# Kernel tuning notes

Hardware: AMD Instinct MI355X
Metric: run time of the kernel (lower is better)

Reference implementation:

```python
import jax, jax.numpy as jnp
import numpy as np

B, S, D, H, KV, HD = 2, 2048, 4096, 32, 8, 128
N_REP = H // KV


def _rope(t, fr, fi):
    # t: [b, s, h, hd]; fr/fi: [s, hd//2] broadcast as [1, s, 1, hd//2]
    t2 = t.reshape(*t.shape[:-1], -1, 2)
    tr, ti = t2[..., 0], t2[..., 1]
    fr = fr[None, :, None, :]
    fi = fi[None, :, None, :]
    orr = tr * fr - fi * ti
    oi = tr * fi + ti * fr
    return jnp.stack([orr, oi], axis=-1).reshape(t.shape)


def setup_inputs() -> dict:
    key = jax.random.key(0)
    ks = jax.random.split(key, 8)
    scale = 0.02
    x = jax.random.normal(ks[0], (B, S, D), jnp.float32)
    wq = jax.random.normal(ks[1], (H * HD, D), jnp.float32) * scale
    wk = jax.random.normal(ks[2], (KV * HD, D), jnp.float32) * scale
    wv = jax.random.normal(ks[3], (KV * HD, D), jnp.float32) * scale
    wo = jax.random.normal(ks[4], (D, H * HD), jnp.float32) * scale
    # rotary frequencies (real/imag parts of freqs_cis)
    t = jnp.arange(S, dtype=jnp.float32)
    inv = 1.0 / (10000.0 ** (jnp.arange(0, HD, 2, dtype=jnp.float32) / HD))
    ang = t[:, None] * inv[None, :]  # [S, HD//2]
    fr, fi = jnp.cos(ang), jnp.sin(ang)
    # causal mask, additive
    mask = jnp.triu(jnp.full((S, S), -1e9, jnp.float32), 1)[None, None]
    cache_k = jnp.zeros((B, S, KV, HD), jnp.float32)
    cache_v = jnp.zeros((B, S, KV, HD), jnp.float32)
    indexes = jnp.arange(S, dtype=jnp.int32)
    cache_indexes = jnp.arange(S, dtype=jnp.int32)
    return dict(x=x, wq=wq, wk=wk, wv=wv, wo=wo, fr=fr, fi=fi, mask=mask,
                cache_k=cache_k, cache_v=cache_v, indexes=indexes,
                cache_indexes=cache_indexes)


def reference(x, wq, wk, wv, wo, fr, fi, mask, cache_k, cache_v, indexes, cache_indexes):
    bsz, seqlen, _ = x.shape
    xq = jnp.einsum('bsd,ed->bse', x, wq).reshape(bsz, seqlen, H, HD)
    xk = jnp.einsum('bsd,ed->bse', x, wk).reshape(bsz, seqlen, KV, HD)
    xv = jnp.einsum('bsd,ed->bse', x, wv).reshape(bsz, seqlen, KV, HD)
    xq = _rope(xq, fr, fi)
    xk = _rope(xk, fr, fi)
    # KV-cache scatter then gather
    cache_k = cache_k.at[:, indexes].set(xk)
    cache_v = cache_v.at[:, indexes].set(xv)
    keys = cache_k[:, cache_indexes]    # [b, kv_len, KV, hd]
    values = cache_v[:, cache_indexes]
    # GQA: repeat_interleave kv heads
    keys = jnp.repeat(keys, N_REP, axis=2)      # [b, kv_len, H, hd]
    values = jnp.repeat(values, N_REP, axis=2)
    q = xq.transpose(0, 2, 1, 3)        # [b, H, s, hd]
    k = keys.transpose(0, 2, 1, 3)      # [b, H, kv, hd]
    v = values.transpose(0, 2, 1, 3)
    scores = jnp.einsum('bhqd,bhkd->bhqk', q, k) / jnp.sqrt(jnp.float32(HD))
    scores = scores + mask
    probs = jax.nn.softmax(scores.astype(jnp.float32), axis=-1).astype(q.dtype)
    out = jnp.einsum('bhqk,bhkd->bhqd', probs, v)
    out = out.transpose(0, 2, 1, 3).reshape(bsz, seqlen, H * HD)
    out = jnp.einsum('bse,de->bsd', out, wo)
    return (out, xk, xv)
```

## Files before the change

### kernel.cpp

```cpp
#include <hip/hip_runtime.h>
#include <hip/hip_bf16.h>


typedef __attribute__((ext_vector_type(8)))  short s8v;
typedef __attribute__((ext_vector_type(4)))  short s4v;
typedef __attribute__((ext_vector_type(4)))  float f4v;
typedef __attribute__((ext_vector_type(16))) float f16v;
typedef __attribute__((ext_vector_type(2)))  float f2v;
typedef __attribute__((ext_vector_type(2))) unsigned int u2v;
typedef __attribute__((ext_vector_type(4))) unsigned int u4v;

typedef __attribute__((address_space(3))) void lds_void;
typedef __attribute__((address_space(1))) void g_void;

#define GLDS16(gp, lp) __builtin_amdgcn_global_load_lds((g_void*)(gp), (lds_void*)(lp), 16, 0, 0)

#define SCL_LOG2 0.12751744f

__device__ __forceinline__ unsigned short f2b(float f) {
  unsigned u = __builtin_bit_cast(unsigned, f);
  u += 0x7fffu + ((u >> 16) & 1u);
  return (unsigned short)(u >> 16);
}
__device__ __forceinline__ unsigned pk2(float a, float b) {
  return (unsigned)f2b(a) | ((unsigned)f2b(b) << 16);
}
__device__ __forceinline__ float b2f(unsigned short h) {
  return __builtin_bit_cast(float, (unsigned)h << 16);
}

__device__ __forceinline__ void mfma32(f4v& d, s8v a, s8v b) {
  asm volatile("v_mfma_f32_16x16x32_bf16 %0, %1, %2, %0" : "+v"(d) : "v"(a), "v"(b));
}
__device__ __forceinline__ void mfma3216(f16v& d, s8v a, s8v b) {
  asm volatile("v_mfma_f32_32x32x16_bf16 %0, %1, %2, %0" : "+v"(d) : "v"(a), "v"(b));
}
__device__ __forceinline__ s4v tr_read(const char* p, int imm) {
  s4v r;
  asm volatile("ds_read_b64_tr_b16 %0, %1 offset:%2"
               : "=v"(r) : "v"((lds_void*)p), "n"(imm));
  return r;
}

__global__ __launch_bounds__(256) void cvt_bf16(const float* __restrict__ s,
                                                unsigned short* __restrict__ d, int n4) {
  const int i = blockIdx.x * 256 + threadIdx.x;
  if (i >= n4) return;
  f4v v = *(const f4v*)(s + (size_t)i * 4);
  u2v r;
  r.x = pk2(v[0], v[1]);
  r.y = pk2(v[2], v[3]);
  *(u2v*)(d + (size_t)i * 4) = r;
}

#define BAR      asm volatile("s_barrier" ::: "memory")
#define WLGKM    do { asm volatile("s_waitcnt lgkmcnt(0)" ::: "memory"); \
                      __builtin_amdgcn_sched_barrier(0); } while (0)
#define WVM8     do { asm volatile("s_waitcnt vmcnt(8)" ::: "memory"); \
                      __builtin_amdgcn_sched_barrier(0); } while (0)

template <int OUTB>
__global__ __launch_bounds__(512, 2) void gemm_bt8(const unsigned short* __restrict__ A,
                                                   const unsigned short* __restrict__ Bp,
                                                   void* __restrict__ Cout,
                                                   int M, int N, int Ks, int Klen,
                                                   int nTiles) {
  __shared__ __align__(16) char smem[131072];
  const int tid = threadIdx.x, lane = tid & 63, wv = tid >> 6;
  const int qi = lane & 15, g = lane >> 4;
  const int wm = wv >> 2, wn = wv & 3;

  const int nwg = gridDim.x, cpx = nwg >> 3;
  const int id = blockIdx.x;
  const int swz = (id & 7) * cpx + (id >> 3);
  const int half = swz / nTiles;
  const int tile = swz - half * nTiles;
  const int kOff = half * Klen;
  const int MT = M >> 8;
  const int m0 = (tile % MT) * 256, n0 = (tile / MT) * 256;
  const int NT = Klen >> 6;

  const int srowo = wv * 8 + (lane >> 3);
  const int scole = ((lane & 7) ^ (lane >> 3)) << 3;
  const size_t rA = (size_t)(m0 + srowo) * Ks + kOff + scole;
  const size_t rB = (size_t)(n0 + srowo) * Ks + kOff + scole;
  char* sdA = smem + wv * 1024;
  char* sdB = smem + 32768 + wv * 1024;

#define STG_A(D, H, KT) do { \
    GLDS16(A + rA + (size_t)((H)*128) * Ks + (size_t)(KT)*64,      sdA + (D)*65536 + (H)*16384); \
    GLDS16(A + rA + (size_t)((H)*128 + 64) * Ks + (size_t)(KT)*64, sdA + (D)*65536 + (H)*16384 + 8192); } while (0)
#define STG_B(D, H, KT) do { \
    GLDS16(Bp + rB + (size_t)((H)*128) * Ks + (size_t)(KT)*64,      sdB + (D)*65536 + (H)*16384); \
    GLDS16(Bp + rB + (size_t)((H)*128 + 64) * Ks + (size_t)(KT)*64, sdB + (D)*65536 + (H)*16384 + 8192); } while (0)

  const int sw = (qi & 7) << 4;
  const char* frA = smem + (wm * 128 + qi) * 128;
  const char* frB = smem + 32768 + (wn * 64 + qi) * 128;

#define RDA4(D, F0) do { _Pragma("unroll") for (int f_ = 0; f_ < 4; ++f_) \
    _Pragma("unroll") for (int k_ = 0; k_ < 2; ++k_) \
      a[(F0) + f_][k_] = *(const s8v*)(frA + (D)*65536 + ((F0) + f_) * 2048 + (((k_ << 6) + (g << 4)) ^ sw)); } while (0)
#define RDB2(D, N0) do { _Pragma("unroll") for (int n_ = 0; n_ < 2; ++n_) \
    _Pragma("unroll") for (int k_ = 0; k_ < 2; ++k_) \
      b[(N0) + n_][k_] = *(const s8v*)(frB + (D)*65536 + ((N0) + n_) * 2048 + (((k_ << 6) + (g << 4)) ^ sw)); } while (0)
#define MQUAD(F0, N0) do { __builtin_amdgcn_s_setprio(1); \
    _Pragma("unroll") for (int f_ = 0; f_ < 4; ++f_) \
    _Pragma("unroll") for (int n_ = 0; n_ < 2; ++n_) \
    _Pragma("unroll") for (int k_ = 0; k_ < 2; ++k_) \
      mfma32(acc[(F0) + f_][(N0) + n_], a[(F0) + f_][k_], b[(N0) + n_][k_]); \
    __builtin_amdgcn_s_setprio(0); } while (0)

  f4v acc[8][4];
#pragma unroll
  for (int i = 0; i < 8; ++i)
#pragma unroll
    for (int j = 0; j < 4; ++j) acc[i][j] = (f4v)0.0f;

  STG_A(0, 0, 0); STG_A(0, 1, 0); STG_B(0, 0, 0); STG_B(0, 1, 0);
  STG_A(1, 0, 1); STG_A(1, 1, 1); STG_B(1, 0, 1); STG_B(1, 1, 1);
  WVM8;
  BAR;

  s8v a[8][2], b[4][2];
#pragma unroll 1
  for (int it = 0; it < NT / 2; ++it) {
    const int t = 2 * it;
    const int k2 = (t + 2 < NT) ? t + 2 : NT - 1;
    const int k3 = (t + 3 < NT) ? t + 3 : NT - 1;
    RDA4(0, 0); RDB2(0, 0);
    WLGKM; MQUAD(0, 0); BAR;
    RDB2(0, 2);
    WLGKM; MQUAD(0, 2); BAR;
    RDA4(0, 4);
    STG_B(0, 0, k2); STG_B(0, 1, k2);
    WLGKM; MQUAD(4, 0); BAR;
    STG_A(0, 0, k2); STG_A(0, 1, k2);
    MQUAD(4, 2);
    WVM8; BAR;
    RDA4(1, 0); RDB2(1, 0);
    WLGKM; MQUAD(0, 0); BAR;
    RDB2(1, 2);
    WLGKM; MQUAD(0, 2); BAR;
    RDA4(1, 4);
    STG_B(1, 0, k3); STG_B(1, 1, k3);
    WLGKM; MQUAD(4, 0); BAR;
    STG_A(1, 0, k3); STG_A(1, 1, k3);
    MQUAD(4, 2);
    WVM8; BAR;
  }

  asm volatile("s_waitcnt vmcnt(0)" ::: "memory");
  asm volatile("s_nop 7\n\ts_nop 7" ::: "memory");
  const int r4 = g * 4;
  if (OUTB) {
    unsigned short* Cb = (unsigned short*)Cout + (size_t)half * M * N;
#pragma unroll
    for (int fm = 0; fm < 8; ++fm)
#pragma unroll
      for (int fn = 0; fn < 4; ++fn)
#pragma unroll
        for (int r = 0; r < 4; ++r)
          Cb[(size_t)(m0 + wm * 128 + fm * 16 + r4 + r) * N + (n0 + wn * 64 + fn * 16 + qi)] =
              f2b(acc[fm][fn][r]);
  } else {
    float* Cf = (float*)Cout;
#pragma unroll
    for (int fm = 0; fm < 8; ++fm)
#pragma unroll
      for (int fn = 0; fn < 4; ++fn)
#pragma unroll
        for (int r = 0; r < 4; ++r)
          Cf[(size_t)(m0 + wm * 128 + fm * 16 + r4 + r) * N + (n0 + wn * 64 + fn * 16 + qi)] =
              acc[fm][fn][r];
  }
}

__global__ __launch_bounds__(256) void rope_scatter(
    const unsigned short* __restrict__ qkvp, const float* __restrict__ fr,
    const float* __restrict__ fi,
    unsigned short* __restrict__ qb, unsigned short* __restrict__ kb,
    unsigned short* __restrict__ vbuf, float* __restrict__ xk, float* __restrict__ xv) {
  const int idx = blockIdx.x * 256 + threadIdx.x;
  const int token = idx / 3072;
  const int col2  = (idx - token * 3072) * 2;
  const int pos   = token & 2047;
  const unsigned u1 = *(const unsigned*)(qkvp + (size_t)token * 6144 + col2);
  const unsigned u2 = *(const unsigned*)(qkvp + 25165824u + (size_t)token * 6144 + col2);
  float v0 = b2f((unsigned short)u1) + b2f((unsigned short)u2);
  float v1 = b2f((unsigned short)(u1 >> 16)) + b2f((unsigned short)(u2 >> 16));
  if (col2 < 4096) {
    const int j = (col2 & 127) >> 1;
    const float cr = fr[pos * 64 + j], ci = fi[pos * 64 + j];
    const float a = (v0 * cr - ci * v1) * SCL_LOG2;
    const float o = (v0 * ci + v1 * cr) * SCL_LOG2;
    *(unsigned*)(qb + (size_t)token * 4096 + col2) = pk2(a, o);
  } else if (col2 < 5120) {
    const int lc = col2 - 4096;
    const int j = (lc & 127) >> 1;
    const float cr = fr[pos * 64 + j], ci = fi[pos * 64 + j];
    const float a = v0 * cr - ci * v1;
    const float o = v0 * ci + v1 * cr;
    *(unsigned*)(kb + (size_t)token * 1024 + lc) = pk2(a, o);
    f2v w; w.x = a; w.y = o;
    *(f2v*)(xk + (size_t)token * 1024 + lc) = w;
  } else {
    const int lc = col2 - 5120;
    *(unsigned*)(vbuf + (size_t)token * 1024 + lc) = pk2(v0, v1);
    f2v w; w.x = v0; w.y = v1;
    *(f2v*)(xv + (size_t)token * 1024 + lc) = w;
  }
}

__global__ __launch_bounds__(512, 2) void attn_fwd(
    const unsigned short* __restrict__ qb, const unsigned short* __restrict__ kb,
    const unsigned short* __restrict__ vb, unsigned short* __restrict__ ao) {
  __shared__ __align__(16) char smem[81920];
  const int tid = threadIdx.x, lane = tid & 63, wv = tid >> 6;
  const int q31 = lane & 31, hi = lane >> 5;
  const int qtb = 7 - blockIdx.x;
  const int h = blockIdx.y, b = blockIdx.z, kvh = h >> 2;
  const int q0 = qtb * 256;
  const int qrow = q0 + wv * 32 + q31;

  s8v qf[8];
  {
    const unsigned short* qp = qb + (size_t)(b * 2048 + qrow) * 4096 + h * 128 + hi * 8;
#pragma unroll
    for (int c = 0; c < 8; ++c) qf[c] = *(const s8v*)(qp + c * 16);
  }

  f16v oacc[4];
#pragma unroll
  for (int i = 0; i < 4; ++i) oacc[i] = (f16v)0.0f;
  float m_run = -3.0e38f, l_run = 0.0f;

  const unsigned short* ksrc[2]; int kdo[2];
#pragma unroll
  for (int j = 0; j < 2; ++j) {
    const int r = wv * 8 + j * 4 + (lane >> 4);
    ksrc[j] = kb + (size_t)(b * 2048 + r) * 1024 + kvh * 128 + (((lane & 15) ^ (r & 15)) << 3);
    kdo[j] = (wv * 8 + j * 4) * 256;
  }
  const unsigned short* vsrc[2]; int vdo[2];
#pragma unroll
  for (int j = 0; j < 2; ++j) {
    const int key = (wv * 2 + j) * 4 + ((lane & 7) >> 1);
    const int d = ((lane >> 3) & 7) * 16 + (lane & 1) * 8;
    vsrc[j] = vb + (size_t)(b * 2048 + key) * 1024 + kvh * 128 + d;
    vdo[j] = (wv * 16 + j * 8) * 128;
  }

  const int ntiles = 4 * qtb + 4;
  const int my_qmax = q0 + wv * 32 + 31, wq_lo = q0 + wv * 32;

  GLDS16(ksrc[0], smem + kdo[0]);
  GLDS16(ksrc[1], smem + kdo[1]);
  GLDS16(ksrc[0] + 65536, smem + 16384 + kdo[0]);
  GLDS16(ksrc[1] + 65536, smem + 16384 + kdo[1]);
  GLDS16(vsrc[0], smem + 49152 + vdo[0]);
  GLDS16(vsrc[1], smem + 49152 + vdo[1]);
  asm volatile("s_waitcnt vmcnt(4)" ::: "memory");
  __builtin_amdgcn_sched_barrier(0);
  BAR;

  int kc = 0;
  for (int t = 0; t < ntiles; ++t) {
    const int k0 = t * 64;
    const bool live = (k0 <= my_qmax);
    const char* Kbase = smem + kc * 16384;
    f16v s32a = (f16v)0.0f, s32b = (f16v)0.0f;
    if (live) {
      __builtin_amdgcn_s_setprio(1);
#pragma unroll
      for (int c = 0; c < 8; ++c) {
        const int sl = ((2 * c + hi) ^ (q31 & 15)) << 4;
        s8v kfa = *(const s8v*)(Kbase + q31 * 256 + sl);
        s8v kfb = *(const s8v*)(Kbase + (32 + q31) * 256 + sl);
        mfma3216(s32a, kfa, qf[c]);
        mfma3216(s32b, kfb, qf[c]);
      }
      __builtin_amdgcn_s_setprio(0);
      asm volatile("s_nop 7\n\ts_nop 7\n\ts_nop 7" : "+v"(s32a), "+v"(s32b));
    }
    {
      const int kt2 = (t + 2 < ntiles) ? t + 2 : ntiles - 1;
      char* kd = smem + ((kc >= 1) ? kc - 1 : 2) * 16384;
      GLDS16(ksrc[0] + (size_t)kt2 * 65536, kd + kdo[0]);
      GLDS16(ksrc[1] + (size_t)kt2 * 65536, kd + kdo[1]);
    }
    asm volatile("s_waitcnt vmcnt(2)" ::: "memory");
    __builtin_amdgcn_sched_barrier(0);
    BAR;
    if (live) {
      const char* vbt = smem + 49152 + (t & 1) * 16384 + hi * 2048 +
                        ((lane >> 4) & 1) * 128 + ((lane & 15) << 3);
      s4v tA[8], tB[8];
#pragma unroll
      for (int u = 0; u < 8; ++u) tA[u] = tr_read(vbt, (u >> 1) * 256 + (u & 1) * 1024);

      float p[32];
#pragma unroll
      for (int r = 0; r < 16; ++r) { p[r] = s32a[r]; p[16 + r] = s32b[r]; }
      float tm = -3.0e38f;
      if (k0 + 64 <= wq_lo) {
#pragma unroll
        for (int j = 0; j < 32; ++j) tm = fmaxf(tm, p[j]);
      } else {
#pragma unroll
        for (int j = 0; j < 32; ++j) {
          const int keyg = k0 + (j >> 4) * 32 + (j & 3) + 8 * ((j >> 2) & 3) + 4 * hi;
          p[j] = (keyg <= qrow) ? p[j] : -3.0e38f;
          tm = fmaxf(tm, p[j]);
        }
      }
      tm = fmaxf(tm, __shfl_xor(tm, 32));

      if (!__all(tm - m_run <= 8.0f)) {
        const float m_new = fmaxf(m_run, tm);
        const float al = exp2f(m_run - m_new);
#pragma unroll
        for (int i = 0; i < 4; ++i)
#pragma unroll
          for (int r = 0; r < 16; ++r) oacc[i][r] *= al;
        l_run *= al;
        m_run = m_new;
      }
      float ps = 0.0f;
#pragma unroll
      for (int j = 0; j < 32; ++j) { p[j] = exp2f(p[j] - m_run); ps += p[j]; }
      ps += __shfl_xor(ps, 32);
      l_run += ps;

      s8v pf[4];
#pragma unroll
      for (int ks = 0; ks < 4; ++ks) {
        unsigned c0, c1, c2, c3;
        asm("v_cvt_pk_bf16_f32 %0, %1, %2" : "=v"(c0) : "v"(p[ks*8+0]), "v"(p[ks*8+1]));
        asm("v_cvt_pk_bf16_f32 %0, %1, %2" : "=v"(c1) : "v"(p[ks*8+2]), "v"(p[ks*8+3]));
        asm("v_cvt_pk_bf16_f32 %0, %1, %2" : "=v"(c2) : "v"(p[ks*8+4]), "v"(p[ks*8+5]));
        asm("v_cvt_pk_bf16_f32 %0, %1, %2" : "=v"(c3) : "v"(p[ks*8+6]), "v"(p[ks*8+7]));
        asm volatile("v_permlane32_swap_b32 %0, %1" : "+v"(c0), "+v"(c2));
        asm volatile("v_permlane32_swap_b32 %0, %1" : "+v"(c1), "+v"(c3));
        u4v pw; pw.x = c0; pw.y = c1; pw.z = c2; pw.w = c3;
        pf[ks] = __builtin_bit_cast(s8v, pw);
      }

#define PVS(KS, CUR, NXT, LAST) do { \
        if (!(LAST)) { \
          _Pragma("unroll") for (int u = 0; u < 8; ++u) \
            NXT[u] = tr_read(vbt, ((KS)+1)*4096 + (u >> 1) * 256 + (u & 1) * 1024); \
          asm volatile("s_waitcnt lgkmcnt(8)" ::: "memory"); \
        } else { asm volatile("s_waitcnt lgkmcnt(0)" ::: "memory"); } \
        __builtin_amdgcn_sched_barrier(0); \
        __builtin_amdgcn_s_setprio(1); \
        _Pragma("unroll") for (int dt = 0; dt < 4; ++dt) { \
          s8v vf = __builtin_shufflevector(CUR[dt*2], CUR[dt*2+1], 0,1,2,3,4,5,6,7); \
          mfma3216(oacc[dt], vf, pf[KS]); } \
        __builtin_amdgcn_s_setprio(0); \
      } while (0)
      PVS(0, tA, tB, 0);
      PVS(1, tB, tA, 0);
      PVS(2, tA, tB, 0);
      PVS(3, tB, tA, 1);
#undef PVS
    }
    {
      const int vt1 = (t + 1 < ntiles) ? t + 1 : ntiles - 1;
      char* vd = smem + 49152 + ((t + 1) & 1) * 16384;
      GLDS16(vsrc[0] + (size_t)vt1 * 65536, vd + vdo[0]);
      GLDS16(vsrc[1] + (size_t)vt1 * 65536, vd + vdo[1]);
    }
    kc = (kc == 2) ? 0 : kc + 1;
  }

  asm volatile("s_waitcnt vmcnt(0) lgkmcnt(0)" ::: "memory");
  asm volatile("s_nop 7\n\ts_nop 7\n\ts_nop 7" ::: "memory");
  __syncthreads();
  const float inv = 1.0f / l_run;
  float* Ost = (float*)smem;
  const int er = tid >> 3, ew = (tid & 7) * 16;
#pragma unroll
  for (int pq = 0; pq < 4; ++pq) {
    if ((wv >> 1) == pq) {
      const int qip = (wv & 1) * 32 + q31;
#pragma unroll
      for (int dt = 0; dt < 4; ++dt)
#pragma unroll
        for (int r = 0; r < 16; ++r) {
          const int d = dt * 32 + (r & 3) + 8 * ((r >> 2) & 3) + 4 * hi;
          Ost[qip * 128 + (d ^ ((qip & 7) << 2))] = oacc[dt][r] * inv;
        }
    }
    __syncthreads();
    const int sw = (er & 7) << 2;
    f4v a0 = *(const f4v*)(Ost + er * 128 + ((ew + 0) ^ sw));
    f4v a1 = *(const f4v*)(Ost + er * 128 + ((ew + 4) ^ sw));
    f4v a2 = *(const f4v*)(Ost + er * 128 + ((ew + 8) ^ sw));
    f4v a3 = *(const f4v*)(Ost + er * 128 + ((ew + 12) ^ sw));
    u4v r0, r1;
    r0.x = pk2(a0[0], a0[1]); r0.y = pk2(a0[2], a0[3]);
    r0.z = pk2(a1[0], a1[1]); r0.w = pk2(a1[2], a1[3]);
    r1.x = pk2(a2[0], a2[1]); r1.y = pk2(a2[2], a2[3]);
    r1.z = pk2(a3[0], a3[1]); r1.w = pk2(a3[2], a3[3]);
    unsigned short* dst = ao + (size_t)(b * 2048 + q0 + pq * 64 + er) * 4096 + h * 128 + ew;
    *(u4v*)dst = r0;
    *(u4v*)(dst + 8) = r1;
    __syncthreads();
  }
}

extern "C" void kernel_launch(void* const* d_in, const int* in_sizes, int n_in,
                              void* d_out, int out_size, void* d_ws, size_t ws_size,
                              hipStream_t stream) {
  (void)in_sizes; (void)n_in; (void)out_size; (void)ws_size;
  const float* x  = (const float*)d_in[0];
  const float* wq = (const float*)d_in[1];
  const float* wk = (const float*)d_in[2];
  const float* wv = (const float*)d_in[3];
  const float* wo = (const float*)d_in[4];
  const float* fr = (const float*)d_in[5];
  const float* fi = (const float*)d_in[6];

  float* out = (float*)d_out;
  float* xk  = out + 16777216;
  float* xv  = xk + 4194304;

  char* ws = (char*)d_ws;
  unsigned short* xb    = (unsigned short*)(ws);
  unsigned short* wqkvb = (unsigned short*)(ws + 33554432);
  unsigned short* wob   = (unsigned short*)(ws + 83886080);
  unsigned short* qkvb  = (unsigned short*)(ws + 117440512);
  unsigned short* aob   = (unsigned short*)(ws + 117440512);
  unsigned short* qbuf  = (unsigned short*)(ws + 218103808);
  unsigned short* kbuf  = (unsigned short*)(ws + 251658240);
  unsigned short* vbuf  = (unsigned short*)(ws + 260046848);

  cvt_bf16<<<16384, 256, 0, stream>>>(x,  xb, 4194304);
  cvt_bf16<<<16384, 256, 0, stream>>>(wq, wqkvb, 4194304);
  cvt_bf16<<<4096,  256, 0, stream>>>(wk, wqkvb + 16777216, 1048576);
  cvt_bf16<<<4096,  256, 0, stream>>>(wv, wqkvb + 20971520, 1048576);
  cvt_bf16<<<16384, 256, 0, stream>>>(wo, wob, 4194304);

  gemm_bt8<1><<<768, 512, 0, stream>>>(xb, wqkvb, qkvb, 4096, 6144, 4096, 2048, 384);
  rope_scatter<<<49152, 256, 0, stream>>>(qkvb, fr, fi, qbuf, kbuf, vbuf, xk, xv);
  attn_fwd<<<dim3(8, 32, 2), 512, 0, stream>>>(qbuf, kbuf, vbuf, aob);
  gemm_bt8<0><<<256, 512, 0, stream>>>(aob, wob, out, 4096, 4096, 4096, 4096, 256);
}
```

Measured before the change: 596.5 us.

## Split causal attention KV range across two blocks and merge partials

Each query tile's key range is split into two halves, each handled by its own block, which doubles the attention grid. Each half writes an unnormalized bf16 partial output and its per-row max and sum. A new merge kernel combines the halves with log-sum-exp weights before the output projection. The aim is to even out the causal load imbalance, where late query tiles have far more key tiles, and to fill more CUs. The cost is an extra kernel launch, extra partial-output memory traffic, and some rounding from storing unnormalized partials in bf16.

Result: slower. 618.1 us (+3.6%).

```diff
diff --git a/kernel.cpp b/kernel.cpp
--- a/kernel.cpp
+++ b/kernel.cpp
@@ -214,14 +214,21 @@
 
 __global__ __launch_bounds__(512, 2) void attn_fwd(
     const unsigned short* __restrict__ qb, const unsigned short* __restrict__ kb,
-    const unsigned short* __restrict__ vb, unsigned short* __restrict__ ao) {
+    const unsigned short* __restrict__ vb, unsigned short* __restrict__ po,
+    float* __restrict__ st) {
   __shared__ __align__(16) char smem[81920];
   const int tid = threadIdx.x, lane = tid & 63, wv = tid >> 6;
   const int q31 = lane & 31, hi = lane >> 5;
-  const int qtb = 7 - blockIdx.x;
+  const int xx = blockIdx.x;
+  const int half = xx & 1;
+  const int qtb = 7 - (xx >> 1);
   const int h = blockIdx.y, b = blockIdx.z, kvh = h >> 2;
   const int q0 = qtb * 256;
   const int qrow = q0 + wv * 32 + q31;
+  const int nt_full = 4 * qtb + 4;
+  const int t0 = half ? (nt_full >> 1) : 0;
+  const int t1 = half ? nt_full : (nt_full >> 1);
+  unsigned short* pout = po + (size_t)half * 16777216u;
 
   s8v qf[8];
   {
@@ -251,21 +258,26 @@
     vdo[j] = (wv * 16 + j * 8) * 128;
   }
 
-  const int ntiles = 4 * qtb + 4;
   const int my_qmax = q0 + wv * 32 + 31, wq_lo = q0 + wv * 32;
 
-  GLDS16(ksrc[0], smem + kdo[0]);
-  GLDS16(ksrc[1], smem + kdo[1]);
-  GLDS16(ksrc[0] + 65536, smem + 16384 + kdo[0]);
-  GLDS16(ksrc[1] + 65536, smem + 16384 + kdo[1]);
-  GLDS16(vsrc[0], smem + 49152 + vdo[0]);
-  GLDS16(vsrc[1], smem + 49152 + vdo[1]);
+  {
+    const int tp1 = (t0 + 1 < t1) ? t0 + 1 : t1 - 1;
+    char* k0d = smem + (t0 % 3) * 16384;
+    char* k1d = smem + ((t0 + 1) % 3) * 16384;
+    char* v0d = smem + 49152 + (t0 & 1) * 16384;
+    GLDS16(ksrc[0] + (size_t)t0 * 65536, k0d + kdo[0]);
+    GLDS16(ksrc[1] + (size_t)t0 * 65536, k0d + kdo[1]);
+    GLDS16(ksrc[0] + (size_t)tp1 * 65536, k1d + kdo[0]);
+    GLDS16(ksrc[1] + (size_t)tp1 * 65536, k1d + kdo[1]);
+    GLDS16(vsrc[0] + (size_t)t0 * 65536, v0d + vdo[0]);
+    GLDS16(vsrc[1] + (size_t)t0 * 65536, v0d + vdo[1]);
+  }
   asm volatile("s_waitcnt vmcnt(4)" ::: "memory");
   __builtin_amdgcn_sched_barrier(0);
   BAR;
 
-  int kc = 0;
-  for (int t = 0; t < ntiles; ++t) {
+  int kc = t0 % 3;
+  for (int t = t0; t < t1; ++t) {
     const int k0 = t * 64;
     const bool live = (k0 <= my_qmax);
     const char* Kbase = smem + kc * 16384;
@@ -284,7 +296,7 @@
       asm volatile("s_nop 7\n\ts_nop 7\n\ts_nop 7" : "+v"(s32a), "+v"(s32b));
     }
     {
-      const int kt2 = (t + 2 < ntiles) ? t + 2 : ntiles - 1;
+      const int kt2 = (t + 2 < t1) ? t + 2 : t1 - 1;
       char* kd = smem + ((kc >= 1) ? kc - 1 : 2) * 16384;
       GLDS16(ksrc[0] + (size_t)kt2 * 65536, kd + kdo[0]);
       GLDS16(ksrc[1] + (size_t)kt2 * 65536, kd + kdo[1]);
@@ -366,7 +378,7 @@
 #undef PVS
     }
     {
-      const int vt1 = (t + 1 < ntiles) ? t + 1 : ntiles - 1;
+      const int vt1 = (t + 1 < t1) ? t + 1 : t1 - 1;
       char* vd = smem + 49152 + ((t + 1) & 1) * 16384;
       GLDS16(vsrc[0] + (size_t)vt1 * 65536, vd + vdo[0]);
       GLDS16(vsrc[1] + (size_t)vt1 * 65536, vd + vdo[1]);
@@ -374,10 +386,16 @@
     kc = (kc == 2) ? 0 : kc + 1;
   }
 
+  if (hi == 0) {
+    float* stp = st + (size_t)half * 262144;
+    const int row = (b * 2048 + q0 + wv * 32 + q31) * 32 + h;
+    f2v s; s.x = m_run; s.y = l_run;
+    *(f2v*)(stp + 2 * (size_t)row) = s;
+  }
+
   asm volatile("s_waitcnt vmcnt(0) lgkmcnt(0)" ::: "memory");
   asm volatile("s_nop 7\n\ts_nop 7\n\ts_nop 7" ::: "memory");
   __syncthreads();
-  const float inv = 1.0f / l_run;
   float* Ost = (float*)smem;
   const int er = tid >> 3, ew = (tid & 7) * 16;
 #pragma unroll
@@ -389,7 +407,7 @@
 #pragma unroll
         for (int r = 0; r < 16; ++r) {
           const int d = dt * 32 + (r & 3) + 8 * ((r >> 2) & 3) + 4 * hi;
-          Ost[qip * 128 + (d ^ ((qip & 7) << 2))] = oacc[dt][r] * inv;
+          Ost[qip * 128 + (d ^ ((qip & 7) << 2))] = oacc[dt][r];
         }
     }
     __syncthreads();
@@ -403,11 +421,38 @@
     r0.z = pk2(a1[0], a1[1]); r0.w = pk2(a1[2], a1[3]);
     r1.x = pk2(a2[0], a2[1]); r1.y = pk2(a2[2], a2[3]);
     r1.z = pk2(a3[0], a3[1]); r1.w = pk2(a3[2], a3[3]);
-    unsigned short* dst = ao + (size_t)(b * 2048 + q0 + pq * 64 + er) * 4096 + h * 128 + ew;
+    unsigned short* dst = pout + (size_t)(b * 2048 + q0 + pq * 64 + er) * 4096 + h * 128 + ew;
     *(u4v*)dst = r0;
     *(u4v*)(dst + 8) = r1;
     __syncthreads();
   }
+}
+
+__global__ __launch_bounds__(256) void attn_merge(
+    const unsigned short* __restrict__ po, const float* __restrict__ st,
+    unsigned short* __restrict__ ao) {
+  const int i = blockIdx.x * 256 + threadIdx.x;
+  const int dg = i & 15;
+  const int row = i >> 4;
+  const f2v s1 = *(const f2v*)(st + 2 * (size_t)row);
+  const f2v s2 = *(const f2v*)(st + 262144 + 2 * (size_t)row);
+  const float M = fmaxf(s1.x, s2.x);
+  const float w1 = exp2f(s1.x - M), w2 = exp2f(s2.x - M);
+  const float inv = 1.0f / (s1.y * w1 + s2.y * w2);
+  const int bq = row >> 5, h = row & 31;
+  const size_t off = (size_t)bq * 4096 + h * 128 + dg * 8;
+  u4v pa = *(const u4v*)(po + off);
+  u4v pb = *(const u4v*)(po + 16777216u + off);
+  u4v r;
+#pragma unroll
+  for (int w = 0; w < 4; ++w) {
+    const unsigned ua = ((unsigned*)&pa)[w], ub = ((unsigned*)&pb)[w];
+    const float lo = (b2f((unsigned short)ua) * w1 + b2f((unsigned short)ub) * w2) * inv;
+    const float hi = (b2f((unsigned short)(ua >> 16)) * w1 +
+                      b2f((unsigned short)(ub >> 16)) * w2) * inv;
+    ((unsigned*)&r)[w] = pk2(lo, hi);
+  }
+  *(u4v*)(ao + off) = r;
 }
 
 extern "C" void kernel_launch(void* const* d_in, const int* in_sizes, int n_in,
@@ -431,7 +476,9 @@
   unsigned short* wqkvb = (unsigned short*)(ws + 33554432);
   unsigned short* wob   = (unsigned short*)(ws + 83886080);
   unsigned short* qkvb  = (unsigned short*)(ws + 117440512);
-  unsigned short* aob   = (unsigned short*)(ws + 117440512);
+  unsigned short* part  = (unsigned short*)(ws + 117440512);
+  float*          stats = (float*)(ws + 188743680);
+  unsigned short* aob   = (unsigned short*)(ws);
   unsigned short* qbuf  = (unsigned short*)(ws + 218103808);
   unsigned short* kbuf  = (unsigned short*)(ws + 251658240);
   unsigned short* vbuf  = (unsigned short*)(ws + 260046848);
@@ -444,6 +491,7 @@
 
   gemm_bt8<1><<<768, 512, 0, stream>>>(xb, wqkvb, qkvb, 4096, 6144, 4096, 2048, 384);
   rope_scatter<<<49152, 256, 0, stream>>>(qkvb, fr, fi, qbuf, kbuf, vbuf, xk, xv);
-  attn_fwd<<<dim3(8, 32, 2), 512, 0, stream>>>(qbuf, kbuf, vbuf, aob);
+  attn_fwd<<<dim3(16, 32, 2), 512, 0, stream>>>(qbuf, kbuf, vbuf, part, stats);
+  attn_merge<<<8192, 256, 0, stream>>>(part, stats, aob);
   gemm_bt8<0><<<256, 512, 0, stream>>>(aob, wob, out, 4096, 4096, 4096, 4096, 256);
 }
```

## Halve attention query tile to 128 rows with 4-wave blocks

Applied to the files above, without the earlier changes.

Each attention block now covers 128 query rows with 4 waves instead of 256 rows with 8 waves, which doubles the grid to 16x32x2. Every wave issues twice as many K/V global-to-LDS loads per tile to keep the staging unchanged, and the epilogue writes 32 columns per thread. The goal is more blocks and better load balance across the causal triangle on the CUs, at the cost of more K/V reloads per query row and fewer waves to hide latency within a block.

Measured after the change: 578.8 us. 1.03x faster.

```diff
diff --git a/kernel.cpp b/kernel.cpp
--- a/kernel.cpp
+++ b/kernel.cpp
@@ -212,15 +212,15 @@
   }
 }
 
-__global__ __launch_bounds__(512, 2) void attn_fwd(
+__global__ __launch_bounds__(256, 2) void attn_fwd(
     const unsigned short* __restrict__ qb, const unsigned short* __restrict__ kb,
     const unsigned short* __restrict__ vb, unsigned short* __restrict__ ao) {
   __shared__ __align__(16) char smem[81920];
   const int tid = threadIdx.x, lane = tid & 63, wv = tid >> 6;
   const int q31 = lane & 31, hi = lane >> 5;
-  const int qtb = 7 - blockIdx.x;
+  const int qtb = 15 - blockIdx.x;
   const int h = blockIdx.y, b = blockIdx.z, kvh = h >> 2;
-  const int q0 = qtb * 256;
+  const int q0 = qtb * 128;
   const int qrow = q0 + wv * 32 + q31;
 
   s8v qf[8];
@@ -235,32 +235,37 @@
   for (int i = 0; i < 4; ++i) oacc[i] = (f16v)0.0f;
   float m_run = -3.0e38f, l_run = 0.0f;
 
-  const unsigned short* ksrc[2]; int kdo[2];
-#pragma unroll
-  for (int j = 0; j < 2; ++j) {
-    const int r = wv * 8 + j * 4 + (lane >> 4);
+  const unsigned short* ksrc[4]; int kdo[4];
+#pragma unroll
+  for (int j = 0; j < 4; ++j) {
+    const int r = wv * 16 + j * 4 + (lane >> 4);
     ksrc[j] = kb + (size_t)(b * 2048 + r) * 1024 + kvh * 128 + (((lane & 15) ^ (r & 15)) << 3);
-    kdo[j] = (wv * 8 + j * 4) * 256;
-  }
-  const unsigned short* vsrc[2]; int vdo[2];
-#pragma unroll
-  for (int j = 0; j < 2; ++j) {
-    const int key = (wv * 2 + j) * 4 + ((lane & 7) >> 1);
+    kdo[j] = (wv * 16 + j * 4) * 256;
+  }
+  const unsigned short* vsrc[4]; int vdo[4];
+#pragma unroll
+  for (int j = 0; j < 4; ++j) {
+    const int key = wv * 16 + j * 4 + ((lane & 7) >> 1);
     const int d = ((lane >> 3) & 7) * 16 + (lane & 1) * 8;
     vsrc[j] = vb + (size_t)(b * 2048 + key) * 1024 + kvh * 128 + d;
-    vdo[j] = (wv * 16 + j * 8) * 128;
-  }
-
-  const int ntiles = 4 * qtb + 4;
+    vdo[j] = (wv * 32 + j * 8) * 128;
+  }
+
+  const int ntiles = 2 * qtb + 2;
   const int my_qmax = q0 + wv * 32 + 31, wq_lo = q0 + wv * 32;
 
-  GLDS16(ksrc[0], smem + kdo[0]);
-  GLDS16(ksrc[1], smem + kdo[1]);
-  GLDS16(ksrc[0] + 65536, smem + 16384 + kdo[0]);
-  GLDS16(ksrc[1] + 65536, smem + 16384 + kdo[1]);
-  GLDS16(vsrc[0], smem + 49152 + vdo[0]);
-  GLDS16(vsrc[1], smem + 49152 + vdo[1]);
-  asm volatile("s_waitcnt vmcnt(4)" ::: "memory");
+  {
+    char* k0d = smem;
+    char* k1d = smem + 16384;
+    char* v0d = smem + 49152;
+#pragma unroll
+    for (int j = 0; j < 4; ++j) GLDS16(ksrc[j], k0d + kdo[j]);
+#pragma unroll
+    for (int j = 0; j < 4; ++j) GLDS16(ksrc[j] + 65536, k1d + kdo[j]);
+#pragma unroll
+    for (int j = 0; j < 4; ++j) GLDS16(vsrc[j], v0d + vdo[j]);
+  }
+  asm volatile("s_waitcnt vmcnt(8)" ::: "memory");
   __builtin_amdgcn_sched_barrier(0);
   BAR;
 
@@ -286,10 +291,10 @@
     {
       const int kt2 = (t + 2 < ntiles) ? t + 2 : ntiles - 1;
       char* kd = smem + ((kc >= 1) ? kc - 1 : 2) * 16384;
-      GLDS16(ksrc[0] + (size_t)kt2 * 65536, kd + kdo[0]);
-      GLDS16(ksrc[1] + (size_t)kt2 * 65536, kd + kdo[1]);
+#pragma unroll
+      for (int j = 0; j < 4; ++j) GLDS16(ksrc[j] + (size_t)kt2 * 65536, kd + kdo[j]);
     }
-    asm volatile("s_waitcnt vmcnt(2)" ::: "memory");
+    asm volatile("s_waitcnt vmcnt(4)" ::: "memory");
     __builtin_amdgcn_sched_barrier(0);
     BAR;
     if (live) {
@@ -368,8 +373,8 @@
     {
       const int vt1 = (t + 1 < ntiles) ? t + 1 : ntiles - 1;
       char* vd = smem + 49152 + ((t + 1) & 1) * 16384;
-      GLDS16(vsrc[0] + (size_t)vt1 * 65536, vd + vdo[0]);
-      GLDS16(vsrc[1] + (size_t)vt1 * 65536, vd + vdo[1]);
+#pragma unroll
+      for (int j = 0; j < 4; ++j) GLDS16(vsrc[j] + (size_t)vt1 * 65536, vd + vdo[j]);
     }
     kc = (kc == 2) ? 0 : kc + 1;
   }
@@ -379,10 +384,10 @@
   __syncthreads();
   const float inv = 1.0f / l_run;
   float* Ost = (float*)smem;
-  const int er = tid >> 3, ew = (tid & 7) * 16;
-#pragma unroll
-  for (int pq = 0; pq < 4; ++pq) {
-    if ((wv >> 1) == pq) {
+  const int er = tid >> 2, ew = (tid & 3) * 32;
+#pragma unroll
+  for (int p = 0; p < 2; ++p) {
+    if ((wv >> 1) == p) {
       const int qip = (wv & 1) * 32 + q31;
 #pragma unroll
       for (int dt = 0; dt < 4; ++dt)
@@ -394,18 +399,25 @@
     }
     __syncthreads();
     const int sw = (er & 7) << 2;
-    f4v a0 = *(const f4v*)(Ost + er * 128 + ((ew + 0) ^ sw));
-    f4v a1 = *(const f4v*)(Ost + er * 128 + ((ew + 4) ^ sw));
-    f4v a2 = *(const f4v*)(Ost + er * 128 + ((ew + 8) ^ sw));
-    f4v a3 = *(const f4v*)(Ost + er * 128 + ((ew + 12) ^ sw));
+    f4v av[8];
+#pragma unroll
+    for (int c = 0; c < 8; ++c)
+      av[c] = *(const f4v*)(Ost + er * 128 + ((ew + c * 4) ^ sw));
     u4v r0, r1;
-    r0.x = pk2(a0[0], a0[1]); r0.y = pk2(a0[2], a0[3]);
-    r0.z = pk2(a1[0], a1[1]); r0.w = pk2(a1[2], a1[3]);
-    r1.x = pk2(a2[0], a2[1]); r1.y = pk2(a2[2], a2[3]);
-    r1.z = pk2(a3[0], a3[1]); r1.w = pk2(a3[2], a3[3]);
-    unsigned short* dst = ao + (size_t)(b * 2048 + q0 + pq * 64 + er) * 4096 + h * 128 + ew;
+    r0.x = pk2(av[0][0], av[0][1]); r0.y = pk2(av[0][2], av[0][3]);
+    r0.z = pk2(av[1][0], av[1][1]); r0.w = pk2(av[1][2], av[1][3]);
+    r1.x = pk2(av[2][0], av[2][1]); r1.y = pk2(av[2][2], av[2][3]);
+    r1.z = pk2(av[3][0], av[3][1]); r1.w = pk2(av[3][2], av[3][3]);
+    u4v r2, r3;
+    r2.x = pk2(av[4][0], av[4][1]); r2.y = pk2(av[4][2], av[4][3]);
+    r2.z = pk2(av[5][0], av[5][1]); r2.w = pk2(av[5][2], av[5][3]);
+    r3.x = pk2(av[6][0], av[6][1]); r3.y = pk2(av[6][2], av[6][3]);
+    r3.z = pk2(av[7][0], av[7][1]); r3.w = pk2(av[7][2], av[7][3]);
+    unsigned short* dst = ao + (size_t)(b * 2048 + q0 + p * 64 + er) * 4096 + h * 128 + ew;
     *(u4v*)dst = r0;
     *(u4v*)(dst + 8) = r1;
+    *(u4v*)(dst + 16) = r2;
+    *(u4v*)(dst + 24) = r3;
     __syncthreads();
   }
 }
@@ -444,6 +456,6 @@
 
   gemm_bt8<1><<<768, 512, 0, stream>>>(xb, wqkvb, qkvb, 4096, 6144, 4096, 2048, 384);
   rope_scatter<<<49152, 256, 0, stream>>>(qkvb, fr, fi, qbuf, kbuf, vbuf, xk, xv);
-  attn_fwd<<<dim3(8, 32, 2), 512, 0, stream>>>(qbuf, kbuf, vbuf, aob);
+  attn_fwd<<<dim3(16, 32, 2), 256, 0, stream>>>(qbuf, kbuf, vbuf, aob);
   gemm_bt8<0><<<256, 512, 0, stream>>>(aob, wob, out, 4096, 4096, 4096, 4096, 256);
 }
```
